# Kernel optimization log

Measured on AMD Instinct MI355X. Metric: run time of the kernel, lower is better.

The kernel has to match this reference:

```python
import jax, jax.numpy as jnp
import numpy as np

N = 200_000
E = 3_200_000
H = 24

def setup_inputs() -> dict:
    key = jax.random.key(0)
    ks = jax.random.split(key, 12)
    s = 1.0 / np.sqrt(H).astype(np.float32)
    u = lambda k, shape: jax.random.uniform(k, shape, jnp.float32, -s, s)
    return {
        "x": jax.random.normal(ks[0], (N,), jnp.float32),
        "h0": jax.random.normal(ks[1], (1, N, H), jnp.float32) * 0.1,
        "c0": jax.random.normal(ks[2], (1, N, H), jnp.float32) * 0.1,
        "edge_index": jax.random.randint(ks[3], (2, E), 0, N, dtype=jnp.int32),
        "w_ih": u(ks[4], (4 * H, 1)),
        "w_hh": u(ks[5], (4 * H, H)),
        "b_ih": u(ks[6], (4 * H,)),
        "b_hh": u(ks[7], (4 * H,)),
        "gcn_w": u(ks[8], (H, H)),
        "gcn_b": u(ks[9], (H,)),
        "lin_w": u(ks[10], (1, H)),
        "lin_b": u(ks[11], (1,)),
    }

def reference(x, h0, c0, edge_index, w_ih, w_hh, b_ih, b_hh, gcn_w, gcn_b, lin_w, lin_b):
    # --- LSTM single step (seq_len=1, batch=N, input_size=1, hidden=H) ---
    h_prev = h0[0]  # [N, H]
    c_prev = c0[0]  # [N, H]
    # gates in torch order: input, forget, cell(g), output
    gates = x[:, None] * w_ih[:, 0][None, :] + b_ih + h_prev @ w_hh.T + b_hh  # [N, 4H]
    i, f, g, o = jnp.split(gates, 4, axis=-1)
    i = jax.nn.sigmoid(i); f = jax.nn.sigmoid(f); o = jax.nn.sigmoid(o); g = jnp.tanh(g)
    c = f * c_prev + i * g
    h = o * jnp.tanh(c)  # [N, H] -- LSTM output == new hidden state

    # --- GCNConv(24,24): symmetric norm with self loops (PyG default) ---
    xw = h @ gcn_w.T  # [N, H]
    src, dst = edge_index[0], edge_index[1]
    deg = jax.ops.segment_sum(jnp.ones(src.shape, xw.dtype), dst, num_segments=N) + 1.0
    dinv = jax.lax.rsqrt(deg)                      # deg >= 1 due to self loops
    norm = dinv[src] * dinv[dst]                   # [E]
    msg = xw[src] * norm[:, None]                  # [E, H]
    agg = jax.ops.segment_sum(msg, dst, num_segments=N)
    agg = agg + xw * (dinv * dinv)[:, None]        # self-loop edges
    conv = agg + gcn_b                             # [N, H]

    # --- Linear(24,1) + elementwise gate ---
    out = (conv @ lin_w.T + lin_b).reshape(-1)     # [N]
    return x * out, h[None], c[None]
```

## Files before the change

kernel.cpp:

```cpp
#include <hip/hip_runtime.h>
#include <math.h>

#define H 24
#define B0 4096
#define B0_SHIFT 12
#define MAXNB 64
#define NBPAD 65
#define REP 4
#define P 8
#define CAP 70000
#define K1_EPB 4096
#define EPT (K1_EPB / 256)

__device__ __forceinline__ float sigmoidf_(float v) {
    return 1.0f / (1.0f + __expf(-v));
}
__device__ __forceinline__ float tanhf_(float v) {
    return 1.0f - 2.0f / (__expf(2.0f * v) + 1.0f);
}

__global__ void init_kernel(unsigned* __restrict__ cursors,
                            const float* __restrict__ gcn_w,
                            const float* __restrict__ gcn_b,
                            const float* __restrict__ lin_w,
                            const float* __restrict__ lin_b,
                            float* __restrict__ g, float* __restrict__ cb, int NB) {
    int t = threadIdx.x;
    if (t < H) {
        float acc = 0.0f;
        for (int j = 0; j < H; j++) acc = fmaf(lin_w[j], gcn_w[j * H + t], acc);
        g[t] = acc;
    }
    if (t == 32) {
        float c = lin_b[0];
        for (int j = 0; j < H; j++) c = fmaf(gcn_b[j], lin_w[j], c);
        *cb = c;
    }
    if (t < MAXNB) cursors[t] = (unsigned)t * CAP;
}

__global__ __launch_bounds__(256) void scatter_kernel(
    const int* __restrict__ src, const int* __restrict__ dst,
    unsigned* __restrict__ cursors, unsigned* __restrict__ pedge, int E, int NB)
{
    __shared__ unsigned cnt[REP * NBPAD];
    __shared__ unsigned rbase[MAXNB];
    __shared__ unsigned c3[MAXNB];
    int start = blockIdx.x * K1_EPB;
    int end   = start + K1_EPB; if (end > E) end = E;
    int rep = threadIdx.x & (REP - 1);

    for (int i = threadIdx.x; i < REP * NBPAD; i += 256) cnt[i] = 0;
    __syncthreads();

    unsigned dreg[EPT];
    #pragma unroll
    for (int q = 0; q < EPT; q++) {
        int e = start + q * 256 + threadIdx.x;
        if (e < end) {
            unsigned d = (unsigned)dst[e];
            dreg[q] = d;
            atomicAdd(&cnt[rep * NBPAD + (d >> B0_SHIFT)], 1u);
        }
    }
    __syncthreads();

    for (int i = threadIdx.x; i < NB; i += 256) {
        unsigned tot = cnt[i] + cnt[NBPAD + i] + cnt[2 * NBPAD + i] + cnt[3 * NBPAD + i];
        rbase[i] = tot ? atomicAdd(&cursors[i], tot) : 0u;
        c3[i] = 0;
    }
    __syncthreads();

    #pragma unroll
    for (int q = 0; q < EPT; q++) {
        int e = start + q * 256 + threadIdx.x;
        if (e < end) {
            unsigned d = dreg[q];
            unsigned b = d >> B0_SHIFT;
            unsigned slot = atomicAdd(&c3[b], 1u);
            unsigned idx  = rbase[b] + slot;
            if (idx < (b + 1u) * CAP)
                pedge[idx] = ((unsigned)src[e] << B0_SHIFT) | (d & (B0 - 1));
        }
    }
}

__global__ __launch_bounds__(256) void deghist_kernel(
    const unsigned* __restrict__ pedge, const unsigned* __restrict__ cursors,
    unsigned short* __restrict__ degp, int NB, int NPAD)
{
    __shared__ unsigned h[B0];
    int b = blockIdx.x % NB, p = blockIdx.x / NB;
    for (int i = threadIdx.x; i < B0; i += 256) h[i] = 0;
    __syncthreads();
    unsigned base = (unsigned)b * CAP;
    unsigned sz = cursors[b] - base; if (sz > CAP) sz = CAP;
    unsigned chunk = (sz + P - 1) / P;
    unsigned s0 = p * chunk;
    unsigned s1 = s0 + chunk; if (s1 > sz) s1 = sz;
    for (unsigned i = s0 + threadIdx.x; i < s1; i += 256)
        atomicAdd(&h[pedge[base + i] & (B0 - 1)], 1u);
    __syncthreads();
    unsigned short* out = degp + (size_t)p * NPAD + (size_t)b * B0;
    for (int i = threadIdx.x; i < B0; i += 256) out[i] = (unsigned short)h[i];
}

__global__ __launch_bounds__(256) void node_kernel(
    const float* __restrict__ x, const float* __restrict__ h0, const float* __restrict__ c0,
    const float* __restrict__ w_ih, const float* __restrict__ w_hh,
    const float* __restrict__ b_ih, const float* __restrict__ b_hh,
    const float* __restrict__ g, const unsigned short* __restrict__ degp, int NPAD,
    float* __restrict__ out_h, float* __restrict__ out_c,
    float* __restrict__ y, float* __restrict__ z, float* __restrict__ dinv, int N)
{
    __shared__ float ws[96 * 24];
    __shared__ float swih[96];
    __shared__ float sbs[96];
    __shared__ float sg[24];

    #pragma unroll 3
    for (int i = threadIdx.x; i < 96 * 24; i += 256) ws[i] = w_hh[i];
    if (threadIdx.x < 96) {
        swih[threadIdx.x] = w_ih[threadIdx.x];
        sbs[threadIdx.x]  = b_ih[threadIdx.x] + b_hh[threadIdx.x];
    } else if (threadIdx.x >= 128 && threadIdx.x < 152) {
        sg[threadIdx.x - 128] = g[threadIdx.x - 128];
    }
    __syncthreads();

    int tid = blockIdx.x * 256 + threadIdx.x;
    int pr  = tid >> 2;
    int n0  = pr * 2;
    if (n0 >= N) return;
    int n1  = n0 + 1;
    int t   = tid & 3;
    int k0  = 6 * t;

    float hp0[H], hp1[H];
    {
        const float4* a4 = (const float4*)(h0 + (size_t)n0 * H);
        const float4* b4 = (const float4*)(h0 + (size_t)n1 * H);
        #pragma unroll
        for (int q = 0; q < 6; q++) {
            float4 va = a4[q], vb = b4[q];
            hp0[4*q+0] = va.x; hp0[4*q+1] = va.y; hp0[4*q+2] = va.z; hp0[4*q+3] = va.w;
            hp1[4*q+0] = vb.x; hp1[4*q+1] = vb.y; hp1[4*q+2] = vb.z; hp1[4*q+3] = vb.w;
        }
    }
    float cp0[6], cp1[6];
    {
        const float2* a2 = (const float2*)(c0 + (size_t)n0 * H + k0);
        const float2* b2 = (const float2*)(c0 + (size_t)n1 * H + k0);
        #pragma unroll
        for (int q = 0; q < 3; q++) {
            float2 va = a2[q], vb = b2[q];
            cp0[2*q] = va.x; cp0[2*q+1] = va.y;
            cp1[2*q] = vb.x; cp1[2*q+1] = vb.y;
        }
    }
    float xv0 = x[n0], xv1 = x[n1];
    float yv0 = 0.0f, yv1 = 0.0f;

    #pragma unroll
    for (int i = 0; i < 6; i++) {
        int k = k0 + i;
        float bi = sbs[k], bf = sbs[k + 24], bg = sbs[k + 48], bo = sbs[k + 72];
        float wik = swih[k], wfk = swih[k + 24], wgk = swih[k + 48], wok = swih[k + 72];
        float gi0 = fmaf(xv0, wik, bi), gi1 = fmaf(xv1, wik, bi);
        float gf0 = fmaf(xv0, wfk, bf), gf1 = fmaf(xv1, wfk, bf);
        float gg0 = fmaf(xv0, wgk, bg), gg1 = fmaf(xv1, wgk, bg);
        float go0 = fmaf(xv0, wok, bo), go1 = fmaf(xv1, wok, bo);
        const float* w0 = ws + k * 24;
        #pragma unroll
        for (int c = 0; c < 6; c++) {
            float4 wi = *(const float4*)(w0 + 4*c);
            float4 wf = *(const float4*)(w0 + 576  + 4*c);
            float4 wg = *(const float4*)(w0 + 1152 + 4*c);
            float4 wo = *(const float4*)(w0 + 1728 + 4*c);
            float a0 = hp0[4*c+0], a1 = hp0[4*c+1], a2 = hp0[4*c+2], a3 = hp0[4*c+3];
            float d0 = hp1[4*c+0], d1 = hp1[4*c+1], d2 = hp1[4*c+2], d3 = hp1[4*c+3];
            gi0 = fmaf(a0, wi.x, gi0); gi0 = fmaf(a1, wi.y, gi0);
            gi0 = fmaf(a2, wi.z, gi0); gi0 = fmaf(a3, wi.w, gi0);
            gi1 = fmaf(d0, wi.x, gi1); gi1 = fmaf(d1, wi.y, gi1);
            gi1 = fmaf(d2, wi.z, gi1); gi1 = fmaf(d3, wi.w, gi1);
            gf0 = fmaf(a0, wf.x, gf0); gf0 = fmaf(a1, wf.y, gf0);
            gf0 = fmaf(a2, wf.z, gf0); gf0 = fmaf(a3, wf.w, gf0);
            gf1 = fmaf(d0, wf.x, gf1); gf1 = fmaf(d1, wf.y, gf1);
            gf1 = fmaf(d2, wf.z, gf1); gf1 = fmaf(d3, wf.w, gf1);
            gg0 = fmaf(a0, wg.x, gg0); gg0 = fmaf(a1, wg.y, gg0);
            gg0 = fmaf(a2, wg.z, gg0); gg0 = fmaf(a3, wg.w, gg0);
            gg1 = fmaf(d0, wg.x, gg1); gg1 = fmaf(d1, wg.y, gg1);
            gg1 = fmaf(d2, wg.z, gg1); gg1 = fmaf(d3, wg.w, gg1);
            go0 = fmaf(a0, wo.x, go0); go0 = fmaf(a1, wo.y, go0);
            go0 = fmaf(a2, wo.z, go0); go0 = fmaf(a3, wo.w, go0);
            go1 = fmaf(d0, wo.x, go1); go1 = fmaf(d1, wo.y, go1);
            go1 = fmaf(d2, wo.z, go1); go1 = fmaf(d3, wo.w, go1);
        }
        gi0 = sigmoidf_(gi0); gf0 = sigmoidf_(gf0); go0 = sigmoidf_(go0); gg0 = tanhf_(gg0);
        gi1 = sigmoidf_(gi1); gf1 = sigmoidf_(gf1); go1 = sigmoidf_(go1); gg1 = tanhf_(gg1);
        float c_0 = fmaf(gf0, cp0[i], gi0 * gg0);
        float c_1 = fmaf(gf1, cp1[i], gi1 * gg1);
        float h_0 = go0 * tanhf_(c_0);
        float h_1 = go1 * tanhf_(c_1);
        out_c[(size_t)n0 * H + k] = c_0;
        out_c[(size_t)n1 * H + k] = c_1;
        out_h[(size_t)n0 * H + k] = h_0;
        out_h[(size_t)n1 * H + k] = h_1;
        float gk = sg[k];
        yv0 = fmaf(h_0, gk, yv0);
        yv1 = fmaf(h_1, gk, yv1);
    }
    yv0 += __shfl_xor(yv0, 1); yv0 += __shfl_xor(yv0, 2);
    yv1 += __shfl_xor(yv1, 1); yv1 += __shfl_xor(yv1, 2);
    if (t < 2) {
        int n = (t == 0) ? n0 : n1;
        float yv = (t == 0) ? yv0 : yv1;
        unsigned dg = 0;
        #pragma unroll
        for (int p = 0; p < P; p++) dg += degp[(size_t)p * NPAD + n];
        float di = rsqrtf((float)dg + 1.0f);
        dinv[n] = di;
        y[n] = yv;
        z[n] = di * yv;
    }
}

__global__ __launch_bounds__(256) void acchist_kernel(
    const unsigned* __restrict__ pedge, const unsigned* __restrict__ cursors,
    const float* __restrict__ z, float* __restrict__ accp, int NB, int NPAD)
{
    __shared__ float h[B0];
    int b = blockIdx.x % NB, p = blockIdx.x / NB;
    for (int i = threadIdx.x; i < B0; i += 256) h[i] = 0.0f;
    __syncthreads();
    unsigned base = (unsigned)b * CAP;
    unsigned sz = cursors[b] - base; if (sz > CAP) sz = CAP;
    unsigned chunk = (sz + P - 1) / P;
    unsigned s0 = p * chunk;
    unsigned s1 = s0 + chunk; if (s1 > sz) s1 = sz;
    for (unsigned i = s0 + threadIdx.x; i < s1; i += 256) {
        unsigned v = pedge[base + i];
        atomicAdd(&h[v & (B0 - 1)], z[v >> B0_SHIFT]);
    }
    __syncthreads();
    float* out = accp + (size_t)p * NPAD + (size_t)b * B0;
    for (int i = threadIdx.x; i < B0; i += 256) out[i] = h[i];
}

__global__ __launch_bounds__(256) void final_kernel(
    const float* __restrict__ x, const float* __restrict__ accp, int NPAD,
    const float* __restrict__ y, const float* __restrict__ dinv,
    const float* __restrict__ cb, float* __restrict__ out, int N)
{
    int n = blockIdx.x * blockDim.x + threadIdx.x;
    if (n >= N) return;
    float a = 0.0f;
    #pragma unroll
    for (int p = 0; p < P; p++) a += accp[(size_t)p * NPAD + n];
    float di = dinv[n];
    float s  = di * a + di * di * y[n] + cb[0];
    out[n] = x[n] * s;
}

extern "C" void kernel_launch(void* const* d_in, const int* in_sizes, int n_in,
                              void* d_out, int out_size, void* d_ws, size_t ws_size,
                              hipStream_t stream) {
    const float* x     = (const float*)d_in[0];
    const float* h0    = (const float*)d_in[1];
    const float* c0    = (const float*)d_in[2];
    const int*   ei    = (const int*)d_in[3];
    const float* w_ih  = (const float*)d_in[4];
    const float* w_hh  = (const float*)d_in[5];
    const float* b_ih  = (const float*)d_in[6];
    const float* b_hh  = (const float*)d_in[7];
    const float* gcn_w = (const float*)d_in[8];
    const float* gcn_b = (const float*)d_in[9];
    const float* lin_w = (const float*)d_in[10];
    const float* lin_b = (const float*)d_in[11];

    const int N = in_sizes[0];
    const int E = in_sizes[3] / 2;
    const int* src = ei;
    const int* dst = ei + E;

    const int NB   = (N + B0 - 1) / B0;
    const int NPAD = NB * B0;

    float* out_gate = (float*)d_out;
    float* out_h    = out_gate + N;
    float* out_c    = out_h + (size_t)N * H;

    char* w = (char*)d_ws;
    unsigned*       pedge   = (unsigned*)w;       w += (size_t)NB * CAP * 4;
    unsigned short* degp    = (unsigned short*)w; w += (size_t)P * NPAD * 2;
    float*          accp    = (float*)w;          w += (size_t)P * NPAD * 4;
    float*          y       = (float*)w;          w += (size_t)N * 4;
    float*          zv      = (float*)w;          w += (size_t)N * 4;
    float*          dinv    = (float*)w;          w += (size_t)N * 4;
    float*          g       = (float*)w;          w += H * 4;
    float*          cb      = (float*)w;          w += 4;
    unsigned*       cursors = (unsigned*)w;       w += MAXNB * 4;

    init_kernel   <<<1, 64, 0, stream>>>(cursors, gcn_w, gcn_b, lin_w, lin_b, g, cb, NB);
    scatter_kernel<<<(E + K1_EPB - 1) / K1_EPB, 256, 0, stream>>>(src, dst, cursors,
                                                                  pedge, E, NB);
    deghist_kernel<<<NB * P, 256, 0, stream>>>(pedge, cursors, degp, NB, NPAD);
    node_kernel   <<<((size_t)(N / 2) * 4 + 255) / 256, 256, 0, stream>>>(
                       x, h0, c0, w_ih, w_hh, b_ih, b_hh, g, degp, NPAD,
                       out_h, out_c, y, zv, dinv, N);
    acchist_kernel<<<NB * P, 256, 0, stream>>>(pedge, cursors, zv, accp, NB, NPAD);
    final_kernel  <<<(N + 255) / 256, 256, 0, stream>>>(x, accp, NPAD, y, dinv, cb,
                                                        out_gate, N);
}
```

Baseline: 114.0 us.

## Process four nodes per LSTM thread group, split degree normalization into separate kernel

The node kernel now has each 4-thread group compute four nodes instead of two, so each shared-memory weight load is reused across more FMAs. Degree summation and the dinv/z computation move out into a new z_kernel, which decouples the LSTM kernel from the degree histogram. The histogram partition count P doubles and the scatter kernel processes fewer edges per block, giving more parallelism. Costs are an extra kernel launch, roughly twice the register use for h_prev (4x24 floats per thread) with possible occupancy loss, and twice as many partial-histogram rows to sum.

```diff
diff --git a/kernel.cpp b/kernel.cpp
--- a/kernel.cpp
+++ b/kernel.cpp
@@ -7,9 +7,9 @@
 #define MAXNB 64
 #define NBPAD 65
 #define REP 4
-#define P 8
+#define P 16
 #define CAP 70000
-#define K1_EPB 4096
+#define K1_EPB 2048
 #define EPT (K1_EPB / 256)
 
 __device__ __forceinline__ float sigmoidf_(float v) {
@@ -110,9 +110,9 @@
     const float* __restrict__ x, const float* __restrict__ h0, const float* __restrict__ c0,
     const float* __restrict__ w_ih, const float* __restrict__ w_hh,
     const float* __restrict__ b_ih, const float* __restrict__ b_hh,
-    const float* __restrict__ g, const unsigned short* __restrict__ degp, int NPAD,
+    const float* __restrict__ g,
     float* __restrict__ out_h, float* __restrict__ out_c,
-    float* __restrict__ y, float* __restrict__ z, float* __restrict__ dinv, int N)
+    float* __restrict__ y, int N)
 {
     __shared__ float ws[96 * 24];
     __shared__ float swih[96];
@@ -130,100 +130,108 @@
     __syncthreads();
 
     int tid = blockIdx.x * 256 + threadIdx.x;
-    int pr  = tid >> 2;
-    int n0  = pr * 2;
+    int grp = tid >> 2;
+    int n0  = grp * 4;
     if (n0 >= N) return;
-    int n1  = n0 + 1;
     int t   = tid & 3;
     int k0  = 6 * t;
 
-    float hp0[H], hp1[H];
+    float hp[4][H];
+    #pragma unroll
+    for (int m = 0; m < 4; m++) {
+        const float4* p4 = (const float4*)(h0 + (size_t)(n0 + m) * H);
+        #pragma unroll
+        for (int q = 0; q < 6; q++) {
+            float4 v = p4[q];
+            hp[m][4*q+0] = v.x; hp[m][4*q+1] = v.y;
+            hp[m][4*q+2] = v.z; hp[m][4*q+3] = v.w;
+        }
+    }
+    float cp[4][6];
+    #pragma unroll
+    for (int m = 0; m < 4; m++) {
+        const float2* c2 = (const float2*)(c0 + (size_t)(n0 + m) * H + k0);
+        #pragma unroll
+        for (int q = 0; q < 3; q++) {
+            float2 v = c2[q];
+            cp[m][2*q] = v.x; cp[m][2*q+1] = v.y;
+        }
+    }
+    float xv[4];
     {
-        const float4* a4 = (const float4*)(h0 + (size_t)n0 * H);
-        const float4* b4 = (const float4*)(h0 + (size_t)n1 * H);
-        #pragma unroll
-        for (int q = 0; q < 6; q++) {
-            float4 va = a4[q], vb = b4[q];
-            hp0[4*q+0] = va.x; hp0[4*q+1] = va.y; hp0[4*q+2] = va.z; hp0[4*q+3] = va.w;
-            hp1[4*q+0] = vb.x; hp1[4*q+1] = vb.y; hp1[4*q+2] = vb.z; hp1[4*q+3] = vb.w;
-        }
-    }
-    float cp0[6], cp1[6];
-    {
-        const float2* a2 = (const float2*)(c0 + (size_t)n0 * H + k0);
-        const float2* b2 = (const float2*)(c0 + (size_t)n1 * H + k0);
-        #pragma unroll
-        for (int q = 0; q < 3; q++) {
-            float2 va = a2[q], vb = b2[q];
-            cp0[2*q] = va.x; cp0[2*q+1] = va.y;
-            cp1[2*q] = vb.x; cp1[2*q+1] = vb.y;
-        }
-    }
-    float xv0 = x[n0], xv1 = x[n1];
-    float yv0 = 0.0f, yv1 = 0.0f;
+        const float4 xq = *(const float4*)(x + n0);
+        xv[0] = xq.x; xv[1] = xq.y; xv[2] = xq.z; xv[3] = xq.w;
+    }
+    float yv[4] = {0.0f, 0.0f, 0.0f, 0.0f};
 
     #pragma unroll
     for (int i = 0; i < 6; i++) {
         int k = k0 + i;
         float bi = sbs[k], bf = sbs[k + 24], bg = sbs[k + 48], bo = sbs[k + 72];
         float wik = swih[k], wfk = swih[k + 24], wgk = swih[k + 48], wok = swih[k + 72];
-        float gi0 = fmaf(xv0, wik, bi), gi1 = fmaf(xv1, wik, bi);
-        float gf0 = fmaf(xv0, wfk, bf), gf1 = fmaf(xv1, wfk, bf);
-        float gg0 = fmaf(xv0, wgk, bg), gg1 = fmaf(xv1, wgk, bg);
-        float go0 = fmaf(xv0, wok, bo), go1 = fmaf(xv1, wok, bo);
+        float gi[4], gf[4], gg[4], go[4];
+        #pragma unroll
+        for (int m = 0; m < 4; m++) {
+            gi[m] = fmaf(xv[m], wik, bi);
+            gf[m] = fmaf(xv[m], wfk, bf);
+            gg[m] = fmaf(xv[m], wgk, bg);
+            go[m] = fmaf(xv[m], wok, bo);
+        }
         const float* w0 = ws + k * 24;
         #pragma unroll
         for (int c = 0; c < 6; c++) {
-            float4 wi = *(const float4*)(w0 + 4*c);
-            float4 wf = *(const float4*)(w0 + 576  + 4*c);
-            float4 wg = *(const float4*)(w0 + 1152 + 4*c);
-            float4 wo = *(const float4*)(w0 + 1728 + 4*c);
-            float a0 = hp0[4*c+0], a1 = hp0[4*c+1], a2 = hp0[4*c+2], a3 = hp0[4*c+3];
-            float d0 = hp1[4*c+0], d1 = hp1[4*c+1], d2 = hp1[4*c+2], d3 = hp1[4*c+3];
-            gi0 = fmaf(a0, wi.x, gi0); gi0 = fmaf(a1, wi.y, gi0);
-            gi0 = fmaf(a2, wi.z, gi0); gi0 = fmaf(a3, wi.w, gi0);
-            gi1 = fmaf(d0, wi.x, gi1); gi1 = fmaf(d1, wi.y, gi1);
-            gi1 = fmaf(d2, wi.z, gi1); gi1 = fmaf(d3, wi.w, gi1);
-            gf0 = fmaf(a0, wf.x, gf0); gf0 = fmaf(a1, wf.y, gf0);
-            gf0 = fmaf(a2, wf.z, gf0); gf0 = fmaf(a3, wf.w, gf0);
-            gf1 = fmaf(d0, wf.x, gf1); gf1 = fmaf(d1, wf.y, gf1);
-            gf1 = fmaf(d2, wf.z, gf1); gf1 = fmaf(d3, wf.w, gf1);
-            gg0 = fmaf(a0, wg.x, gg0); gg0 = fmaf(a1, wg.y, gg0);
-            gg0 = fmaf(a2, wg.z, gg0); gg0 = fmaf(a3, wg.w, gg0);
-            gg1 = fmaf(d0, wg.x, gg1); gg1 = fmaf(d1, wg.y, gg1);
-            gg1 = fmaf(d2, wg.z, gg1); gg1 = fmaf(d3, wg.w, gg1);
-            go0 = fmaf(a0, wo.x, go0); go0 = fmaf(a1, wo.y, go0);
-            go0 = fmaf(a2, wo.z, go0); go0 = fmaf(a3, wo.w, go0);
-            go1 = fmaf(d0, wo.x, go1); go1 = fmaf(d1, wo.y, go1);
-            go1 = fmaf(d2, wo.z, go1); go1 = fmaf(d3, wo.w, go1);
-        }
-        gi0 = sigmoidf_(gi0); gf0 = sigmoidf_(gf0); go0 = sigmoidf_(go0); gg0 = tanhf_(gg0);
-        gi1 = sigmoidf_(gi1); gf1 = sigmoidf_(gf1); go1 = sigmoidf_(go1); gg1 = tanhf_(gg1);
-        float c_0 = fmaf(gf0, cp0[i], gi0 * gg0);
-        float c_1 = fmaf(gf1, cp1[i], gi1 * gg1);
-        float h_0 = go0 * tanhf_(c_0);
-        float h_1 = go1 * tanhf_(c_1);
-        out_c[(size_t)n0 * H + k] = c_0;
-        out_c[(size_t)n1 * H + k] = c_1;
-        out_h[(size_t)n0 * H + k] = h_0;
-        out_h[(size_t)n1 * H + k] = h_1;
-        float gk = sg[k];
-        yv0 = fmaf(h_0, gk, yv0);
-        yv1 = fmaf(h_1, gk, yv1);
-    }
-    yv0 += __shfl_xor(yv0, 1); yv0 += __shfl_xor(yv0, 2);
-    yv1 += __shfl_xor(yv1, 1); yv1 += __shfl_xor(yv1, 2);
-    if (t < 2) {
-        int n = (t == 0) ? n0 : n1;
-        float yv = (t == 0) ? yv0 : yv1;
-        unsigned dg = 0;
-        #pragma unroll
-        for (int p = 0; p < P; p++) dg += degp[(size_t)p * NPAD + n];
-        float di = rsqrtf((float)dg + 1.0f);
-        dinv[n] = di;
-        y[n] = yv;
-        z[n] = di * yv;
-    }
+            float4 wi4 = *(const float4*)(w0 + 4*c);
+            float4 wf4 = *(const float4*)(w0 + 576  + 4*c);
+            float4 wg4 = *(const float4*)(w0 + 1152 + 4*c);
+            float4 wo4 = *(const float4*)(w0 + 1728 + 4*c);
+            #pragma unroll
+            for (int m = 0; m < 4; m++) {
+                float a0 = hp[m][4*c+0], a1 = hp[m][4*c+1];
+                float a2 = hp[m][4*c+2], a3 = hp[m][4*c+3];
+                gi[m] = fmaf(a0, wi4.x, gi[m]); gi[m] = fmaf(a1, wi4.y, gi[m]);
+                gi[m] = fmaf(a2, wi4.z, gi[m]); gi[m] = fmaf(a3, wi4.w, gi[m]);
+                gf[m] = fmaf(a0, wf4.x, gf[m]); gf[m] = fmaf(a1, wf4.y, gf[m]);
+                gf[m] = fmaf(a2, wf4.z, gf[m]); gf[m] = fmaf(a3, wf4.w, gf[m]);
+                gg[m] = fmaf(a0, wg4.x, gg[m]); gg[m] = fmaf(a1, wg4.y, gg[m]);
+                gg[m] = fmaf(a2, wg4.z, gg[m]); gg[m] = fmaf(a3, wg4.w, gg[m]);
+                go[m] = fmaf(a0, wo4.x, go[m]); go[m] = fmaf(a1, wo4.y, go[m]);
+                go[m] = fmaf(a2, wo4.z, go[m]); go[m] = fmaf(a3, wo4.w, go[m]);
+            }
+        }
+        #pragma unroll
+        for (int m = 0; m < 4; m++) {
+            float giv = sigmoidf_(gi[m]);
+            float gfv = sigmoidf_(gf[m]);
+            float gov = sigmoidf_(go[m]);
+            float ggv = tanhf_(gg[m]);
+            float c_ = fmaf(gfv, cp[m][i], giv * ggv);
+            float h_ = gov * tanhf_(c_);
+            out_c[(size_t)(n0 + m) * H + k] = c_;
+            out_h[(size_t)(n0 + m) * H + k] = h_;
+            yv[m] = fmaf(h_, sg[k], yv[m]);
+        }
+    }
+    #pragma unroll
+    for (int m = 0; m < 4; m++) {
+        yv[m] += __shfl_xor(yv[m], 1);
+        yv[m] += __shfl_xor(yv[m], 2);
+    }
+    float yout = (t == 0) ? yv[0] : (t == 1) ? yv[1] : (t == 2) ? yv[2] : yv[3];
+    y[n0 + t] = yout;
+}
+
+__global__ __launch_bounds__(256) void z_kernel(
+    const float* __restrict__ y, const unsigned short* __restrict__ degp, int NPAD,
+    float* __restrict__ dinv, float* __restrict__ z, int N)
+{
+    int n = blockIdx.x * 256 + threadIdx.x;
+    if (n >= N) return;
+    unsigned dg = 0;
+    #pragma unroll
+    for (int p = 0; p < P; p++) dg += degp[(size_t)p * NPAD + n];
+    float di = rsqrtf((float)dg + 1.0f);
+    dinv[n] = di;
+    z[n] = di * y[n];
 }
 
 __global__ __launch_bounds__(256) void acchist_kernel(
@@ -306,9 +314,9 @@
     scatter_kernel<<<(E + K1_EPB - 1) / K1_EPB, 256, 0, stream>>>(src, dst, cursors,
                                                                   pedge, E, NB);
     deghist_kernel<<<NB * P, 256, 0, stream>>>(pedge, cursors, degp, NB, NPAD);
-    node_kernel   <<<((size_t)(N / 2) * 4 + 255) / 256, 256, 0, stream>>>(
-                       x, h0, c0, w_ih, w_hh, b_ih, b_hh, g, degp, NPAD,
-                       out_h, out_c, y, zv, dinv, N);
+    node_kernel   <<<(N + 255) / 256, 256, 0, stream>>>(x, h0, c0, w_ih, w_hh, b_ih, b_hh,
+                                                        g, out_h, out_c, y, N);
+    z_kernel      <<<(N + 255) / 256, 256, 0, stream>>>(y, degp, NPAD, dinv, zv, N);
     acchist_kernel<<<NB * P, 256, 0, stream>>>(pedge, cursors, zv, accp, NB, NPAD);
     final_kernel  <<<(N + 255) / 256, 256, 0, stream>>>(x, accp, NPAD, y, dinv, cb,
                                                         out_gate, N);
```

After: 134.1 us. +17.6%, slower.
